# Performance work log

Hardware: AMD Instinct MI355X
Metric: run time of the kernel (lower is better)

Reference implementation:

```python
import jax, jax.numpy as jnp
import numpy as np

D = 1024       # d_model
H = 16         # nhead
DFF = 4096     # dim_feedforward
TM = 512       # T_motion (seq_len)
TA = 512       # T_audio
B = 32         # batch
NBEATS = 64
SIGMA = 4.0    # temporal_sigma
BW = 2.0       # beat_weight
LN_EPS = 1e-5


def setup_inputs() -> dict:
    key = jax.random.key(0)
    ks = jax.random.split(key, 12)
    p = lambda k, shape: jax.random.normal(k, shape, jnp.float32) * 0.02
    return {
        "src": jax.random.normal(ks[0], (TM, B, D), jnp.float32),
        "audio_memory": jax.random.normal(ks[1], (TA, B, D), jnp.float32),
        "beat_frames": jax.random.randint(ks[2], (NBEATS,), 0, TA),
        # self-attention (packed in_proj like nn.MultiheadAttention)
        "sa_in_w": p(ks[3], (3 * D, D)), "sa_in_b": jnp.zeros((3 * D,), jnp.float32),
        "sa_out_w": p(ks[4], (D, D)), "sa_out_b": jnp.zeros((D,), jnp.float32),
        # cross-attention
        "ca_in_w": p(ks[5], (3 * D, D)), "ca_in_b": jnp.zeros((3 * D,), jnp.float32),
        "ca_out_w": p(ks[6], (D, D)), "ca_out_b": jnp.zeros((D,), jnp.float32),
        "gate": jnp.array(0.5, jnp.float32),  # cross_attn_gate (nonzero so branch is active)
        # layernorms
        "n1_g": jnp.ones((D,), jnp.float32), "n1_b": jnp.zeros((D,), jnp.float32),
        "nc_g": jnp.ones((D,), jnp.float32), "nc_b": jnp.zeros((D,), jnp.float32),
        "n2_g": jnp.ones((D,), jnp.float32), "n2_b": jnp.zeros((D,), jnp.float32),
        # FFN
        "lin1_w": p(ks[7], (DFF, D)), "lin1_b": jnp.zeros((DFF,), jnp.float32),
        "lin2_w": p(ks[8], (D, DFF)), "lin2_b": jnp.zeros((D,), jnp.float32),
    }


def _layernorm(x, g, b):
    m = jnp.mean(x, axis=-1, keepdims=True)
    v = jnp.var(x, axis=-1, keepdims=True)
    return (x - m) * jax.lax.rsqrt(v + LN_EPS) * g + b


def _mha(q, k, v, w_in, b_in, w_out, b_out, bias=None):
    # q: (Tq,B,D), k/v: (Tk,B,D); packed in_proj like nn.MultiheadAttention
    hd = D // H
    wq, wk, wv = jnp.split(w_in, 3, axis=0)
    bq, bk, bv = jnp.split(b_in, 3, axis=0)
    def proj(x, w, bb):  # (T,B,D) -> (B,H,T,hd)
        y = jnp.einsum('tbd,ed->tbe', x, w) + bb
        return y.reshape(y.shape[0], y.shape[1], H, hd).transpose(1, 2, 0, 3)
    qh, kh, vh = proj(q, wq, bq), proj(k, wk, bk), proj(v, wv, bv)
    scores = jnp.einsum('bhqd,bhkd->bhqk', qh, kh) / jnp.sqrt(jnp.float32(hd))
    if bias is not None:
        scores = scores + bias[None, None]  # (Tq,Tk) broadcast over (B,H)
    attn = jax.nn.softmax(scores, axis=-1)
    o = jnp.einsum('bhqk,bhkd->bhqd', attn, vh)          # (B,H,Tq,hd)
    o = o.transpose(2, 0, 1, 3).reshape(q.shape[0], q.shape[1], D)  # (Tq,B,D)
    return jnp.einsum('tbd,ed->tbe', o, w_out) + b_out


def _temporal_bias(t_motion, t_audio, sigma):
    scale = (t_audio - 1) / (t_motion - 1) if (t_motion > 1 and t_audio > 1) else 1.0
    audio_pos = jnp.arange(t_motion, dtype=jnp.float32) * scale
    diff = audio_pos[:, None] - jnp.arange(t_audio, dtype=jnp.float32)[None, :]
    return -(diff ** 2) / (2.0 * sigma ** 2)  # (T_motion, T_audio)


def _beat_bias(t_audio, beats, bw):
    # equivalent to sequential torch loop: beat position -> bw, neighbors -> max(., bw/2)
    bias = jnp.zeros((t_audio,), jnp.float32)
    l_idx = jnp.where(beats > 0, beats - 1, 0)
    l_val = jnp.where(beats > 0, bw * 0.5, 0.0)
    r_idx = jnp.where(beats < t_audio - 1, beats + 1, t_audio - 1)
    r_val = jnp.where(beats < t_audio - 1, bw * 0.5, 0.0)
    bias = bias.at[l_idx].max(l_val).at[r_idx].max(r_val).at[beats].max(bw)
    return bias


def reference(src, audio_memory, beat_frames, sa_in_w, sa_in_b, sa_out_w, sa_out_b,
              ca_in_w, ca_in_b, ca_out_w, ca_out_b, gate,
              n1_g, n1_b, nc_g, nc_b, n2_g, n2_b,
              lin1_w, lin1_b, lin2_w, lin2_b):
    # self-attention + residual + LN (dropout is identity in eval)
    x = src + _mha(src, src, src, sa_in_w, sa_in_b, sa_out_w, sa_out_b)
    x = _layernorm(x, n1_g, n1_b)
    # biased cross-attention to audio
    bias = _temporal_bias(TM, TA, SIGMA) + _beat_bias(TA, beat_frames, BW)[None, :]
    cross = _mha(x, audio_memory, audio_memory, ca_in_w, ca_in_b, ca_out_w, ca_out_b, bias)
    x = x + jnp.tanh(gate) * cross
    x = _layernorm(x, nc_g, nc_b)
    # FFN
    h = jax.nn.gelu(jnp.einsum('tbd,fd->tbf', x, lin1_w) + lin1_b, approximate=False)
    ff = jnp.einsum('tbf,df->tbd', h, lin2_w) + lin2_b
    x = _layernorm(x + ff, n2_g, n2_b)
    return x
```

## Files before the change

kernel.cpp:

```cpp
#include <hip/hip_runtime.h>
#include <hip/hip_bf16.h>

#define D_MODEL 1024
#define NHEAD   16
#define HDIM    64
#define DFF_    4096
#define TM_     512
#define TA_     512
#define BATCH   32
#define NTOK    (TM_ * BATCH)
#define NBEATS_ 64

typedef __bf16 bfv8 __attribute__((ext_vector_type(8)));
typedef float  f32x4 __attribute__((ext_vector_type(4)));
typedef unsigned short u16x8 __attribute__((ext_vector_type(8)));
typedef unsigned short u16x4 __attribute__((ext_vector_type(4)));

__device__ __forceinline__ unsigned short f2bf(float f) {
  union { float f; unsigned u; } v; v.f = f;
  unsigned r = v.u + 0x7fffu + ((v.u >> 16) & 1u);
  return (unsigned short)(r >> 16);
}
__device__ __forceinline__ float bf2f(unsigned short h) {
  union { unsigned u; float f; } v; v.u = ((unsigned)h) << 16;
  return v.f;
}
__device__ __forceinline__ unsigned pk2bf(float a, float b) {
  __hip_bfloat162 t = __float22bfloat162_rn(make_float2(a, b));
  union { __hip_bfloat162 h; unsigned u; } v; v.h = t;
  return v.u;
}
__device__ __forceinline__ float gelu_fast(float v) {
  float t = v * v;
  float e = __expf(v * fmaf(0.0713554f, t, 1.5957691f));
  float r = __builtin_amdgcn_rcpf(e + 1.0f);
  return v - v * r;
}

#define GLOAD_LDS16(g, l) __builtin_amdgcn_global_load_lds( \
    (const __attribute__((address_space(1))) unsigned int*)(g), \
    (__attribute__((address_space(3))) unsigned int*)(l), 16, 0, 0)

#define MEMFENCE asm volatile("" ::: "memory")
#define BARRIER  do { MEMFENCE; __builtin_amdgcn_s_barrier(); MEMFENCE; } while (0)

__global__ __launch_bounds__(256) void copy_f32(const float* __restrict__ in, float* __restrict__ out) {
  long i = ((long)blockIdx.x * 256 + threadIdx.x) * 4;
  *(float4*)(out + i) = *(const float4*)(in + i);
}

__global__ __launch_bounds__(256) void cvt_f32_bf16(
    const float* __restrict__ in, unsigned short* __restrict__ out) {
  long i = ((long)blockIdx.x * 256 + threadIdx.x) * 4;
  float4 v = *(const float4*)(in + i);
  u16x4 o = { f2bf(v.x), f2bf(v.y), f2bf(v.z), f2bf(v.w) };
  *(u16x4*)(out + i) = o;
}

__global__ __launch_bounds__(256) void cvt_remap_bt(
    const float* __restrict__ in, unsigned short* __restrict__ out) {
  long rin = blockIdx.x;
  int b = (int)(rin & 31), t = (int)(rin >> 5);
  long rout = (long)b * 512 + t;
  int c = threadIdx.x * 4;
  float4 v = *(const float4*)(in + rin * 1024 + c);
  u16x4 o = { f2bf(v.x), f2bf(v.y), f2bf(v.z), f2bf(v.w) };
  *(u16x4*)(out + rout * 1024 + c) = o;
}

__global__ __launch_bounds__(512) void build_biasT(
    const int* __restrict__ beats, float* __restrict__ biasT) {
  int ta = blockIdx.x;
  int tm = threadIdx.x;
  float m = 0.f;
  for (int i = 0; i < NBEATS_; ++i) {
    int bf = beats[i];
    if (bf == ta) m = fmaxf(m, 2.0f);
    if (bf > 0 && bf - 1 == ta) m = fmaxf(m, 1.0f);
    if (bf < TA_ - 1 && bf + 1 == ta) m = fmaxf(m, 1.0f);
  }
  float diff = (float)tm - (float)ta;
  biasT[ta * TM_ + tm] = -(diff * diff) * (1.0f / 32.0f) + m;
}

template<int EPI, int SWAP>
__global__ __launch_bounds__(512, 2) void gemm256p(
    const unsigned short* __restrict__ A, const unsigned short* __restrict__ Bw,
    const float* __restrict__ bias, int K,
    unsigned short* __restrict__ outP, int ldc,
    unsigned short* __restrict__ dq, unsigned short* __restrict__ dk,
    unsigned short* __restrict__ dv, int s1) {
  __shared__ __align__(16) unsigned short As[2][2][128 * 64];
  __shared__ __align__(16) unsigned short Bs[2][2][128 * 64];
  const int tid = threadIdx.x;
  const int w = tid >> 6, lane = tid & 63;
  const int l15 = lane & 15, l4 = lane >> 4;
  const int wm = w >> 2, wn = w & 3;
  const long m0 = (long)blockIdx.x * 256;
  const long n0 = (long)blockIdx.y * 256;
  const int srow8 = lane >> 3;
  const int scol = ((lane & 7) ^ srow8) * 8;

  const unsigned short* bA00 = A  + (m0 +       (w * 2 + 0) * 8 + srow8) * (long)K + scol;
  const unsigned short* bA01 = A  + (m0 +       (w * 2 + 1) * 8 + srow8) * (long)K + scol;
  const unsigned short* bA10 = A  + (m0 + 128 + (w * 2 + 0) * 8 + srow8) * (long)K + scol;
  const unsigned short* bA11 = A  + (m0 + 128 + (w * 2 + 1) * 8 + srow8) * (long)K + scol;
  const unsigned short* bB00 = Bw + (n0 +       (w * 2 + 0) * 8 + srow8) * (long)K + scol;
  const unsigned short* bB01 = Bw + (n0 +       (w * 2 + 1) * 8 + srow8) * (long)K + scol;
  const unsigned short* bB10 = Bw + (n0 + 128 + (w * 2 + 0) * 8 + srow8) * (long)K + scol;
  const unsigned short* bB11 = Bw + (n0 + 128 + (w * 2 + 1) * 8 + srow8) * (long)K + scol;

  auto stA = [&](int kt, int h, const unsigned short* p0, const unsigned short* p1) {
    const int db = kt & 1;
    const long ko = (long)kt * 64;
    GLOAD_LDS16(p0 + ko, &As[db][h][(w * 2 + 0) * 512]);
    GLOAD_LDS16(p1 + ko, &As[db][h][(w * 2 + 1) * 512]);
  };
  auto stB = [&](int kt, int h, const unsigned short* p0, const unsigned short* p1) {
    const int db = kt & 1;
    const long ko = (long)kt * 64;
    GLOAD_LDS16(p0 + ko, &Bs[db][h][(w * 2 + 0) * 512]);
    GLOAD_LDS16(p1 + ko, &Bs[db][h][(w * 2 + 1) * 512]);
  };
  const int swzb0 = ((l4)     ^ (l15 & 7)) << 4;
  const int swzb1 = ((l4 + 4) ^ (l15 & 7)) << 4;
  auto rdfrag = [&](const unsigned short* buf, int r, int kk) -> bfv8 {
    return *(const bfv8*)((const char*)buf + r * 128 + (kk ? swzb1 : swzb0));
  };

  f32x4 acc[8][4] = {};
  bfv8 aF[4][2], bF[4][2];
  const int nt = K >> 6;
  const int hB = wn >> 1, rB0 = (wn & 1) * 64;

  stA(0, 0, bA00, bA01); stA(0, 1, bA10, bA11);
  stB(0, 0, bB00, bB01); stB(0, 1, bB10, bB11);
  stB(1, 0, bB00, bB01); stB(1, 1, bB10, bB11);
  stA(1, 0, bA00, bA01); stA(1, 1, bA10, bA11);
  asm volatile("s_waitcnt vmcnt(8)" ::: "memory");
  BARRIER;

  for (int t = 0; t < nt; ++t) {
    const int db = t & 1;
    const unsigned short* Ah = &As[db][wm][0];
    const unsigned short* Bh = &Bs[db][hB][0];
    const bool pf2 = (t + 2 < nt);

#pragma unroll
    for (int mf = 0; mf < 4; ++mf) {
      aF[mf][0] = rdfrag(Ah, mf * 16 + l15, 0);
      aF[mf][1] = rdfrag(Ah, mf * 16 + l15, 1);
    }
#pragma unroll
    for (int nf = 0; nf < 2; ++nf) {
      bF[nf][0] = rdfrag(Bh, rB0 + nf * 16 + l15, 0);
      bF[nf][1] = rdfrag(Bh, rB0 + nf * 16 + l15, 1);
    }
    BARRIER;
    asm volatile("s_waitcnt lgkmcnt(0)" ::: "memory");
    __builtin_amdgcn_s_setprio(1);
#pragma unroll
    for (int mf = 0; mf < 4; ++mf)
#pragma unroll
      for (int nf = 0; nf < 2; ++nf)
#pragma unroll
        for (int kk = 0; kk < 2; ++kk)
          acc[mf][nf] = SWAP
            ? __builtin_amdgcn_mfma_f32_16x16x32_bf16(bF[nf][kk], aF[mf][kk], acc[mf][nf], 0, 0, 0)
            : __builtin_amdgcn_mfma_f32_16x16x32_bf16(aF[mf][kk], bF[nf][kk], acc[mf][nf], 0, 0, 0);
    __builtin_amdgcn_s_setprio(0);
    BARRIER;

#pragma unroll
    for (int nf = 2; nf < 4; ++nf) {
      bF[nf][0] = rdfrag(Bh, rB0 + nf * 16 + l15, 0);
      bF[nf][1] = rdfrag(Bh, rB0 + nf * 16 + l15, 1);
    }
    BARRIER;
    asm volatile("s_waitcnt lgkmcnt(0)" ::: "memory");
    __builtin_amdgcn_s_setprio(1);
#pragma unroll
    for (int mf = 0; mf < 4; ++mf)
#pragma unroll
      for (int nf = 2; nf < 4; ++nf)
#pragma unroll
        for (int kk = 0; kk < 2; ++kk)
          acc[mf][nf] = SWAP
            ? __builtin_amdgcn_mfma_f32_16x16x32_bf16(bF[nf][kk], aF[mf][kk], acc[mf][nf], 0, 0, 0)
            : __builtin_amdgcn_mfma_f32_16x16x32_bf16(aF[mf][kk], bF[nf][kk], acc[mf][nf], 0, 0, 0);
    __builtin_amdgcn_s_setprio(0);
    BARRIER;

#pragma unroll
    for (int mf = 0; mf < 4; ++mf) {
      aF[mf][0] = rdfrag(Ah, (mf + 4) * 16 + l15, 0);
      aF[mf][1] = rdfrag(Ah, (mf + 4) * 16 + l15, 1);
    }
    if (pf2) { stB(t + 2, 0, bB00, bB01); stB(t + 2, 1, bB10, bB11); }
    BARRIER;
    asm volatile("s_waitcnt lgkmcnt(0)" ::: "memory");
    __builtin_amdgcn_s_setprio(1);
#pragma unroll
    for (int mf = 0; mf < 4; ++mf)
#pragma unroll
      for (int nf = 0; nf < 2; ++nf)
#pragma unroll
        for (int kk = 0; kk < 2; ++kk)
          acc[mf + 4][nf] = SWAP
            ? __builtin_amdgcn_mfma_f32_16x16x32_bf16(bF[nf][kk], aF[mf][kk], acc[mf + 4][nf], 0, 0, 0)
            : __builtin_amdgcn_mfma_f32_16x16x32_bf16(aF[mf][kk], bF[nf][kk], acc[mf + 4][nf], 0, 0, 0);
    __builtin_amdgcn_s_setprio(0);
    BARRIER;

    if (pf2) { stA(t + 2, 0, bA00, bA01); stA(t + 2, 1, bA10, bA11); }
    __builtin_amdgcn_s_setprio(1);
#pragma unroll
    for (int mf = 0; mf < 4; ++mf)
#pragma unroll
      for (int nf = 2; nf < 4; ++nf)
#pragma unroll
        for (int kk = 0; kk < 2; ++kk)
          acc[mf + 4][nf] = SWAP
            ? __builtin_amdgcn_mfma_f32_16x16x32_bf16(bF[nf][kk], aF[mf][kk], acc[mf + 4][nf], 0, 0, 0)
            : __builtin_amdgcn_mfma_f32_16x16x32_bf16(aF[mf][kk], bF[nf][kk], acc[mf + 4][nf], 0, 0, 0);
    __builtin_amdgcn_s_setprio(0);
    if (pf2)                asm volatile("s_waitcnt vmcnt(8)" ::: "memory");
    else if (t + 1 < nt)    asm volatile("s_waitcnt vmcnt(0)" ::: "memory");
    BARRIER;
  }

#pragma unroll
  for (int mf = 0; mf < 8; ++mf)
#pragma unroll
    for (int nf = 0; nf < 4; ++nf) {
      if (SWAP) {
        const int mrow = (int)m0 + wm * 128 + mf * 16 + l15;
        const int col0 = (int)n0 + wn * 64 + nf * 16 + l4 * 4;
        float4 bv = bias ? *(const float4*)&bias[col0] : make_float4(0.f, 0.f, 0.f, 0.f);
        float v0 = acc[mf][nf][0] + bv.x, v1 = acc[mf][nf][1] + bv.y;
        float v2 = acc[mf][nf][2] + bv.z, v3 = acc[mf][nf][3] + bv.w;
        if (EPI == 1) { v0 = gelu_fast(v0); v1 = gelu_fast(v1); v2 = gelu_fast(v2); v3 = gelu_fast(v3); }
        if (EPI == 0 || EPI == 1) {
          uint2 ov; ov.x = pk2bf(v0, v1); ov.y = pk2bf(v2, v3);
          *(uint2*)&outP[(long)mrow * ldc + col0] = ov;
        } else {
          int b_ = mrow >> 9, t_ = mrow & 511;
          if (col0 < s1) {
            int h = col0 >> 6, d0 = col0 & 63;
            uint2 ov; ov.x = pk2bf(v0 * 0.125f, v1 * 0.125f); ov.y = pk2bf(v2 * 0.125f, v3 * 0.125f);
            *(uint2*)&dq[(((long)b_ * NHEAD + h) * TM_ + t_) * HDIM + d0] = ov;
          } else {
            int c0 = col0 - s1, h = c0 >> 6, d0 = c0 & 63;
            uint2 ov; ov.x = pk2bf(v0, v1); ov.y = pk2bf(v2, v3);
            *(uint2*)&dk[(((long)b_ * NHEAD + h) * TA_ + t_) * HDIM + d0] = ov;
          }
        }
      } else {
        const int col = (int)n0 + wn * 64 + nf * 16 + l15;
        const int row0 = (int)m0 + wm * 128 + mf * 16 + l4 * 4;
        float bv = bias ? bias[col] : 0.f;
        int b_ = row0 >> 9, t0 = row0 & 511;
        int h = col >> 6, d = col & 63;
        uint2 ov;
        ov.x = pk2bf(acc[mf][nf][0] + bv, acc[mf][nf][1] + bv);
        ov.y = pk2bf(acc[mf][nf][2] + bv, acc[mf][nf][3] + bv);
        *(uint2*)&dv[(((long)b_ * NHEAD + h) * HDIM + d) * TA_ + t0] = ov;
      }
    }
}

template<int BIAS>
__global__ __launch_bounds__(512) void attn_fused8(
    const unsigned short* __restrict__ Qr, const unsigned short* __restrict__ Kr,
    const unsigned short* __restrict__ Vt, const float* __restrict__ biasT,
    unsigned short* __restrict__ Orow) {
  __shared__ __align__(16) unsigned short Kb[2][64 * 64];
  __shared__ __align__(16) unsigned short Vb[2][64 * 64];
  __shared__ __align__(16) unsigned short P_lds[8][16][64];
  const int flat = blockIdx.y * 4 + blockIdx.x;
  const int W = (flat & 7) * 256 + (flat >> 3);
  const int bh = W >> 2;
  const int b = bh >> 4, h = bh & 15;
  const int tid = threadIdx.x, w = tid >> 6, lane = tid & 63;
  const int l15 = lane & 15, l4 = lane >> 4;
  const int q0 = (W & 3) * 128 + w * 16;

  const unsigned short* Kg = Kr + (long)bh * TA_ * HDIM;
  const unsigned short* Vg = Vt + (long)bh * HDIM * TA_;

  const int stg_row = lane >> 3;
  const int stg_col = ((lane & 7) ^ stg_row) * 8;

  auto stage = [&](int t, int cb) {
    const int kv0 = t * 64;
    int row = w * 8 + stg_row;
    GLOAD_LDS16(Kg + (long)(kv0 + row) * HDIM + stg_col, &Kb[cb][(w * 8) * 64]);
    GLOAD_LDS16(Vg + (long)row * TA_ + kv0 + stg_col,    &Vb[cb][(w * 8) * 64]);
  };

  bfv8 qf[2];
#pragma unroll
  for (int kc = 0; kc < 2; ++kc)
    qf[kc] = *(const bfv8*)&Qr[((long)bh * TM_ + q0 + l15) * HDIM + kc * 32 + l4 * 8];

  float mrun = -1e30f, lrun = 0.f;
  f32x4 o[4] = {};
  unsigned short* prow = &P_lds[w][l15][0];
  const int swz = (l15 & 7) * 8;

  stage(0, 0);
  __syncthreads();
  int cur = 0;

  for (int t = 0; t < 8; ++t) {
    if (t < 7) stage(t + 1, cur ^ 1);
    const int kv0 = t * 64;
    f32x4 s[4] = {};
#pragma unroll
    for (int f = 0; f < 4; ++f) {
#pragma unroll
      for (int kc = 0; kc < 2; ++kc) {
        bfv8 kf = *(const bfv8*)&Kb[cur][(f * 16 + l15) * 64 + (((kc * 4 + l4) * 8) ^ swz)];
        s[f] = __builtin_amdgcn_mfma_f32_16x16x32_bf16(kf, qf[kc], s[f], 0, 0, 0);
      }
    }
    if (BIAS) {
#pragma unroll
      for (int f = 0; f < 4; ++f)
#pragma unroll
        for (int r = 0; r < 4; ++r)
          s[f][r] += biasT[(long)(kv0 + f * 16 + l4 * 4 + r) * TM_ + q0 + l15];
    }
    float t0 = fmaxf(fmaxf(s[0][0], s[0][1]), fmaxf(s[0][2], s[0][3]));
    float t1 = fmaxf(fmaxf(s[1][0], s[1][1]), fmaxf(s[1][2], s[1][3]));
    float t2 = fmaxf(fmaxf(s[2][0], s[2][1]), fmaxf(s[2][2], s[2][3]));
    float t3 = fmaxf(fmaxf(s[3][0], s[3][1]), fmaxf(s[3][2], s[3][3]));
    float pmax = fmaxf(fmaxf(t0, t1), fmaxf(t2, t3));
    pmax = fmaxf(pmax, __shfl_xor(pmax, 16));
    pmax = fmaxf(pmax, __shfl_xor(pmax, 32));
    if (!__all(pmax - mrun <= 8.0f)) {
      float newm = fmaxf(mrun, pmax);
      float corr = __expf(mrun - newm);
      lrun *= corr;
#pragma unroll
      for (int fd = 0; fd < 4; ++fd)
#pragma unroll
        for (int r = 0; r < 4; ++r) o[fd][r] *= corr;
      mrun = newm;
    }
    float p0 = 0.f, p1 = 0.f, p2 = 0.f, p3 = 0.f;
#pragma unroll
    for (int f = 0; f < 4; ++f) {
      float e0 = __expf(s[f][0] - mrun), e1 = __expf(s[f][1] - mrun);
      float e2 = __expf(s[f][2] - mrun), e3 = __expf(s[f][3] - mrun);
      p0 += e0; p1 += e1; p2 += e2; p3 += e3;
      unsigned w0 = pk2bf(e0, e1);
      unsigned w1 = pk2bf(e2, e3);
      int blkW = ((f << 1) | (l4 >> 1)) ^ (l15 & 7);
      uint2 pw; pw.x = w0; pw.y = w1;
      *(uint2*)((char*)prow + blkW * 16 + (l4 & 1) * 8) = pw;
    }
    float psum = (p0 + p1) + (p2 + p3);
    psum += __shfl_xor(psum, 16);
    psum += __shfl_xor(psum, 32);
    lrun += psum;
    asm volatile("s_waitcnt lgkmcnt(0)" ::: "memory");
    __builtin_amdgcn_sched_barrier(0);
#pragma unroll
    for (int c = 0; c < 2; ++c) {
      int blkR = ((c << 2) | l4) ^ (l15 & 7);
      bfv8 pa = *(const bfv8*)((const char*)prow + blkR * 16);
#pragma unroll
      for (int fd = 0; fd < 4; ++fd) {
        bfv8 vb = *(const bfv8*)&Vb[cur][(fd * 16 + l15) * 64 + (((c * 4 + l4) * 8) ^ swz)];
        o[fd] = __builtin_amdgcn_mfma_f32_16x16x32_bf16(vb, pa, o[fd], 0, 0, 0);
      }
    }
    __syncthreads();
    cur ^= 1;
  }

  float invl = 1.f / lrun;
  const long obase = ((long)b * 512 + q0 + l15) * D_MODEL + h * HDIM;
#pragma unroll
  for (int fd = 0; fd < 4; ++fd) {
    uint2 ov;
    ov.x = pk2bf(o[fd][0] * invl, o[fd][1] * invl);
    ov.y = pk2bf(o[fd][2] * invl, o[fd][3] * invl);
    *(uint2*)&Orow[obase + fd * 16 + l4 * 4] = ov;
  }
}

__global__ __launch_bounds__(256) void ln_fused(
    const unsigned short* __restrict__ cin,
    const float* __restrict__ residf, const unsigned short* __restrict__ residb,
    const float* __restrict__ gamma, const float* __restrict__ beta,
    const float* __restrict__ gate,
    float* __restrict__ out_f32, unsigned short* __restrict__ out_bf16,
    int remap_resid, int remap_out) {
  long row = blockIdx.x;
  int t = threadIdx.x;
  int tt = (int)(row & 511), bb = (int)(row >> 9);
  long row_tb = (long)tt * 32 + bb;
  float gf = gate ? tanhf(gate[0]) : 1.0f;
  u16x4 cvb = *(const u16x4*)(cin + row * 1024 + t * 4);
  float c0 = bf2f(cvb[0]), c1 = bf2f(cvb[1]), c2 = bf2f(cvb[2]), c3 = bf2f(cvb[3]);
  float r0, r1, r2, r3;
  if (residf) {
    long rr = remap_resid ? row_tb : row;
    float4 rv = *(const float4*)(residf + rr * 1024 + t * 4);
    r0 = rv.x; r1 = rv.y; r2 = rv.z; r3 = rv.w;
  } else {
    u16x4 rv = *(const u16x4*)(residb + row * 1024 + t * 4);
    r0 = bf2f(rv[0]); r1 = bf2f(rv[1]); r2 = bf2f(rv[2]); r3 = bf2f(rv[3]);
  }
  float y0 = r0 + gf * c0, y1 = r1 + gf * c1, y2 = r2 + gf * c2, y3 = r3 + gf * c3;
  float s = y0 + y1 + y2 + y3;
  float q = y0 * y0 + y1 * y1 + y2 * y2 + y3 * y3;
#pragma unroll
  for (int off = 32; off; off >>= 1) { s += __shfl_xor(s, off); q += __shfl_xor(q, off); }
  __shared__ float sw[4], qw[4];
  int wave = t >> 6;
  if ((t & 63) == 0) { sw[wave] = s; qw[wave] = q; }
  __syncthreads();
  s = sw[0] + sw[1] + sw[2] + sw[3];
  q = qw[0] + qw[1] + qw[2] + qw[3];
  float mean = s * (1.0f / 1024.0f);
  float var = q * (1.0f / 1024.0f) - mean * mean;
  float rstd = rsqrtf(var + 1e-5f);
  float4 g4 = *(const float4*)(gamma + t * 4);
  float4 b4 = *(const float4*)(beta + t * 4);
  float o0 = (y0 - mean) * rstd * g4.x + b4.x;
  float o1 = (y1 - mean) * rstd * g4.y + b4.y;
  float o2 = (y2 - mean) * rstd * g4.z + b4.z;
  float o3 = (y3 - mean) * rstd * g4.w + b4.w;
  if (out_f32) {
    long ro = remap_out ? row_tb : row;
    float4 o = { o0, o1, o2, o3 };
    *(float4*)(out_f32 + ro * 1024 + t * 4) = o;
  }
  if (out_bf16) {
    u16x4 ob = { f2bf(o0), f2bf(o1), f2bf(o2), f2bf(o3) };
    *(u16x4*)(out_bf16 + row * 1024 + t * 4) = ob;
  }
}

static inline char* wsa(char*& p, size_t bytes) {
  char* r = p;
  p += (bytes + 255) & ~(size_t)255;
  return r;
}

extern "C" void kernel_launch(void* const* d_in, const int* in_sizes, int n_in,
                              void* d_out, int out_size, void* d_ws, size_t ws_size,
                              hipStream_t stream) {
  const float* src      = (const float*)d_in[0];
  const float* audio    = (const float*)d_in[1];
  const int*   beats    = (const int*)d_in[2];
  const float* sa_in_w  = (const float*)d_in[3];
  const float* sa_in_b  = (const float*)d_in[4];
  const float* sa_out_w = (const float*)d_in[5];
  const float* sa_out_b = (const float*)d_in[6];
  const float* ca_in_w  = (const float*)d_in[7];
  const float* ca_in_b  = (const float*)d_in[8];
  const float* ca_out_w = (const float*)d_in[9];
  const float* ca_out_b = (const float*)d_in[10];
  const float* gate     = (const float*)d_in[11];
  const float* n1_g     = (const float*)d_in[12];
  const float* n1_b     = (const float*)d_in[13];
  const float* nc_g     = (const float*)d_in[14];
  const float* nc_b     = (const float*)d_in[15];
  const float* n2_g     = (const float*)d_in[16];
  const float* n2_b     = (const float*)d_in[17];
  const float* l1_w     = (const float*)d_in[18];
  const float* l1_b     = (const float*)d_in[19];
  const float* l2_w     = (const float*)d_in[20];
  const float* l2_b     = (const float*)d_in[21];
  float* out = (float*)d_out;
  (void)in_sizes; (void)n_in; (void)out_size;

  const size_t NEEDED = (size_t)236000000;
  if (ws_size < NEEDED) {
    copy_f32<<<dim3(NTOK), dim3(256), 0, stream>>>(src, out);
    return;
  }

  char* p = (char*)d_ws;
  float*          biasT  = (float*)         wsa(p, (size_t)TM_ * TA_ * 4);
  unsigned short* wsaiw  = (unsigned short*)wsa(p, (size_t)3 * D_MODEL * D_MODEL * 2);
  unsigned short* wsaow  = (unsigned short*)wsa(p, (size_t)D_MODEL * D_MODEL * 2);
  unsigned short* wcaiw  = (unsigned short*)wsa(p, (size_t)3 * D_MODEL * D_MODEL * 2);
  unsigned short* wcaow  = (unsigned short*)wsa(p, (size_t)D_MODEL * D_MODEL * 2);
  unsigned short* wl1    = (unsigned short*)wsa(p, (size_t)DFF_ * D_MODEL * 2);
  unsigned short* wl2    = (unsigned short*)wsa(p, (size_t)D_MODEL * DFF_ * 2);
  unsigned short* srcb   = (unsigned short*)wsa(p, (size_t)NTOK * D_MODEL * 2);
  unsigned short* audb   = (unsigned short*)wsa(p, (size_t)NTOK * D_MODEL * 2);
  unsigned short* Qr     = (unsigned short*)wsa(p, (size_t)NTOK * D_MODEL * 2);
  unsigned short* Kr     = (unsigned short*)wsa(p, (size_t)NTOK * D_MODEL * 2);
  unsigned short* Vt     = (unsigned short*)wsa(p, (size_t)NTOK * D_MODEL * 2);
  unsigned short* x1b    = (unsigned short*)wsa(p, (size_t)NTOK * D_MODEL * 2);
  unsigned short* Orow   = srcb;
  unsigned short* C1     = Vt;
  unsigned short* x2b    = audb;
  unsigned short* H1     = Qr;
  unsigned short* C2     = srcb;

  build_biasT<<<dim3(TA_), dim3(TM_), 0, stream>>>(beats, biasT);
  cvt_remap_bt<<<dim3(NTOK), dim3(256), 0, stream>>>(src, srcb);
  cvt_remap_bt<<<dim3(NTOK), dim3(256), 0, stream>>>(audio, audb);
  cvt_f32_bf16<<<dim3((3 * D_MODEL * D_MODEL) / 1024), dim3(256), 0, stream>>>(sa_in_w, wsaiw);
  cvt_f32_bf16<<<dim3((D_MODEL * D_MODEL) / 1024), dim3(256), 0, stream>>>(sa_out_w, wsaow);
  cvt_f32_bf16<<<dim3((3 * D_MODEL * D_MODEL) / 1024), dim3(256), 0, stream>>>(ca_in_w, wcaiw);
  cvt_f32_bf16<<<dim3((D_MODEL * D_MODEL) / 1024), dim3(256), 0, stream>>>(ca_out_w, wcaow);
  cvt_f32_bf16<<<dim3((DFF_ * D_MODEL) / 1024), dim3(256), 0, stream>>>(l1_w, wl1);
  cvt_f32_bf16<<<dim3((D_MODEL * DFF_) / 1024), dim3(256), 0, stream>>>(l2_w, wl2);

  gemm256p<3, 1><<<dim3(64, 8), dim3(512), 0, stream>>>(
      srcb, wsaiw, sa_in_b, 1024, nullptr, 0, Qr, Kr, nullptr, 1024);
  gemm256p<2, 0><<<dim3(64, 4), dim3(512), 0, stream>>>(
      srcb, wsaiw + (size_t)2048 * D_MODEL, sa_in_b + 2048, 1024,
      nullptr, 0, nullptr, nullptr, Vt, 0);
  attn_fused8<0><<<dim3(TM_ / 128, BATCH * NHEAD), dim3(512), 0, stream>>>(Qr, Kr, Vt, nullptr, Orow);
  gemm256p<0, 1><<<dim3(64, 4), dim3(512), 0, stream>>>(
      Orow, wsaow, sa_out_b, 1024, C1, 1024, nullptr, nullptr, nullptr, 0);
  ln_fused<<<dim3(NTOK), dim3(256), 0, stream>>>(
      C1, src, nullptr, n1_g, n1_b, nullptr, nullptr, x1b, 1, 0);

  gemm256p<3, 1><<<dim3(64, 4), dim3(512), 0, stream>>>(
      x1b, wcaiw, ca_in_b, 1024, nullptr, 0, Qr, nullptr, nullptr, 1024);
  gemm256p<3, 1><<<dim3(64, 4), dim3(512), 0, stream>>>(
      audb, wcaiw + (size_t)1024 * D_MODEL, ca_in_b + 1024, 1024,
      nullptr, 0, nullptr, Kr, nullptr, 0);
  gemm256p<2, 0><<<dim3(64, 4), dim3(512), 0, stream>>>(
      audb, wcaiw + (size_t)2048 * D_MODEL, ca_in_b + 2048, 1024,
      nullptr, 0, nullptr, nullptr, Vt, 0);
  attn_fused8<1><<<dim3(TM_ / 128, BATCH * NHEAD), dim3(512), 0, stream>>>(Qr, Kr, Vt, biasT, Orow);
  gemm256p<0, 1><<<dim3(64, 4), dim3(512), 0, stream>>>(
      Orow, wcaow, ca_out_b, 1024, C1, 1024, nullptr, nullptr, nullptr, 0);
  ln_fused<<<dim3(NTOK), dim3(256), 0, stream>>>(
      C1, nullptr, x1b, nc_g, nc_b, gate, nullptr, x2b, 0, 0);

  gemm256p<1, 1><<<dim3(64, 16), dim3(512), 0, stream>>>(
      x2b, wl1, l1_b, 1024, H1, DFF_, nullptr, nullptr, nullptr, 0);
  gemm256p<0, 1><<<dim3(64, 4), dim3(512), 0, stream>>>(
      H1, wl2, l2_b, DFF_, C2, 1024, nullptr, nullptr, nullptr, 0);
  ln_fused<<<dim3(NTOK), dim3(256), 0, stream>>>(
      C2, nullptr, x2b, n2_g, n2_b, nullptr, out, nullptr, 0, 1);
}
```

Before: 1.008 ms.

## Triple-buffer attention K/V staging with one barrier and row-major bias loads

The attention kernel moves from a double-buffered K/V staging loop with two __syncthreads per tile to a three-slot ring. Loads are issued two tiles ahead, and each step uses explicit vmcnt waits plus a single barrier. This is meant to hide global-load latency and cut synchronisation. The temporal/beat bias table is also stored query-major, so each lane reads its bias as float4 vector loads instead of sixteen strided scalar loads. The extra LDS buffer raises shared-memory use per block, and the vmcnt counts depend on the assumption that stage issues exactly two loads.

```diff
diff --git a/kernel.cpp b/kernel.cpp
--- a/kernel.cpp
+++ b/kernel.cpp
@@ -68,10 +68,10 @@
   *(u16x4*)(out + rout * 1024 + c) = o;
 }
 
-__global__ __launch_bounds__(512) void build_biasT(
-    const int* __restrict__ beats, float* __restrict__ biasT) {
-  int ta = blockIdx.x;
-  int tm = threadIdx.x;
+__global__ __launch_bounds__(512) void build_bias(
+    const int* __restrict__ beats, float* __restrict__ bias2d) {
+  int tm = blockIdx.x;
+  int ta = threadIdx.x;
   float m = 0.f;
   for (int i = 0; i < NBEATS_; ++i) {
     int bf = beats[i];
@@ -80,7 +80,7 @@
     if (bf < TA_ - 1 && bf + 1 == ta) m = fmaxf(m, 1.0f);
   }
   float diff = (float)tm - (float)ta;
-  biasT[ta * TM_ + tm] = -(diff * diff) * (1.0f / 32.0f) + m;
+  bias2d[(long)tm * TA_ + ta] = -(diff * diff) * (1.0f / 32.0f) + m;
 }
 
 template<int EPI, int SWAP>
@@ -270,12 +270,12 @@
 }
 
 template<int BIAS>
-__global__ __launch_bounds__(512) void attn_fused8(
+__global__ __launch_bounds__(512) void attn_fused9(
     const unsigned short* __restrict__ Qr, const unsigned short* __restrict__ Kr,
-    const unsigned short* __restrict__ Vt, const float* __restrict__ biasT,
+    const unsigned short* __restrict__ Vt, const float* __restrict__ bias2d,
     unsigned short* __restrict__ Orow) {
-  __shared__ __align__(16) unsigned short Kb[2][64 * 64];
-  __shared__ __align__(16) unsigned short Vb[2][64 * 64];
+  __shared__ __align__(16) unsigned short Kb[3][64 * 64];
+  __shared__ __align__(16) unsigned short Vb[3][64 * 64];
   __shared__ __align__(16) unsigned short P_lds[8][16][64];
   const int flat = blockIdx.y * 4 + blockIdx.x;
   const int W = (flat & 7) * 256 + (flat >> 3);
@@ -307,13 +307,17 @@
   f32x4 o[4] = {};
   unsigned short* prow = &P_lds[w][l15][0];
   const int swz = (l15 & 7) * 8;
+  const float* biasrow = BIAS ? &bias2d[(long)(q0 + l15) * TA_] : nullptr;
 
   stage(0, 0);
-  __syncthreads();
-  int cur = 0;
+  stage(1, 1);
 
   for (int t = 0; t < 8; ++t) {
-    if (t < 7) stage(t + 1, cur ^ 1);
+    if (t < 7) asm volatile("s_waitcnt vmcnt(2)" ::: "memory");
+    else       asm volatile("s_waitcnt vmcnt(0)" ::: "memory");
+    BARRIER;
+    if (t + 2 < 8) stage(t + 2, (t + 2) % 3);
+    const int cur = t % 3;
     const int kv0 = t * 64;
     f32x4 s[4] = {};
 #pragma unroll
@@ -326,10 +330,10 @@
     }
     if (BIAS) {
 #pragma unroll
-      for (int f = 0; f < 4; ++f)
-#pragma unroll
-        for (int r = 0; r < 4; ++r)
-          s[f][r] += biasT[(long)(kv0 + f * 16 + l4 * 4 + r) * TM_ + q0 + l15];
+      for (int f = 0; f < 4; ++f) {
+        float4 bv = *(const float4*)&biasrow[kv0 + f * 16 + l4 * 4];
+        s[f][0] += bv.x; s[f][1] += bv.y; s[f][2] += bv.z; s[f][3] += bv.w;
+      }
     }
     float t0 = fmaxf(fmaxf(s[0][0], s[0][1]), fmaxf(s[0][2], s[0][3]));
     float t1 = fmaxf(fmaxf(s[1][0], s[1][1]), fmaxf(s[1][2], s[1][3]));
@@ -376,8 +380,6 @@
         o[fd] = __builtin_amdgcn_mfma_f32_16x16x32_bf16(vb, pa, o[fd], 0, 0, 0);
       }
     }
-    __syncthreads();
-    cur ^= 1;
   }
 
   float invl = 1.f / lrun;
@@ -486,7 +488,7 @@
   }
 
   char* p = (char*)d_ws;
-  float*          biasT  = (float*)         wsa(p, (size_t)TM_ * TA_ * 4);
+  float*          bias2d = (float*)         wsa(p, (size_t)TM_ * TA_ * 4);
   unsigned short* wsaiw  = (unsigned short*)wsa(p, (size_t)3 * D_MODEL * D_MODEL * 2);
   unsigned short* wsaow  = (unsigned short*)wsa(p, (size_t)D_MODEL * D_MODEL * 2);
   unsigned short* wcaiw  = (unsigned short*)wsa(p, (size_t)3 * D_MODEL * D_MODEL * 2);
@@ -505,7 +507,7 @@
   unsigned short* H1     = Qr;
   unsigned short* C2     = srcb;
 
-  build_biasT<<<dim3(TA_), dim3(TM_), 0, stream>>>(beats, biasT);
+  build_bias<<<dim3(TM_), dim3(TA_), 0, stream>>>(beats, bias2d);
   cvt_remap_bt<<<dim3(NTOK), dim3(256), 0, stream>>>(src, srcb);
   cvt_remap_bt<<<dim3(NTOK), dim3(256), 0, stream>>>(audio, audb);
   cvt_f32_bf16<<<dim3((3 * D_MODEL * D_MODEL) / 1024), dim3(256), 0, stream>>>(sa_in_w, wsaiw);
@@ -520,7 +522,7 @@
   gemm256p<2, 0><<<dim3(64, 4), dim3(512), 0, stream>>>(
       srcb, wsaiw + (size_t)2048 * D_MODEL, sa_in_b + 2048, 1024,
       nullptr, 0, nullptr, nullptr, Vt, 0);
-  attn_fused8<0><<<dim3(TM_ / 128, BATCH * NHEAD), dim3(512), 0, stream>>>(Qr, Kr, Vt, nullptr, Orow);
+  attn_fused9<0><<<dim3(TM_ / 128, BATCH * NHEAD), dim3(512), 0, stream>>>(Qr, Kr, Vt, nullptr, Orow);
   gemm256p<0, 1><<<dim3(64, 4), dim3(512), 0, stream>>>(
       Orow, wsaow, sa_out_b, 1024, C1, 1024, nullptr, nullptr, nullptr, 0);
   ln_fused<<<dim3(NTOK), dim3(256), 0, stream>>>(
@@ -534,7 +536,7 @@
   gemm256p<2, 0><<<dim3(64, 4), dim3(512), 0, stream>>>(
       audb, wcaiw + (size_t)2048 * D_MODEL, ca_in_b + 2048, 1024,
       nullptr, 0, nullptr, nullptr, Vt, 0);
-  attn_fused8<1><<<dim3(TM_ / 128, BATCH * NHEAD), dim3(512), 0, stream>>>(Qr, Kr, Vt, biasT, Orow);
+  attn_fused9<1><<<dim3(TM_ / 128, BATCH * NHEAD), dim3(512), 0, stream>>>(Qr, Kr, Vt, bias2d, Orow);
   gemm256p<0, 1><<<dim3(64, 4), dim3(512), 0, stream>>>(
       Orow, wcaow, ca_out_b, 1024, C1, 1024, nullptr, nullptr, nullptr, 0);
   ln_fused<<<dim3(NTOK), dim3(256), 0, stream>>>(
```

After: 946.3 us. 6.2% less time.
